# Kernel optimization log

Hardware: AMD Instinct MI355X
Metric: run time of the kernel (lower is better)

The kernel has to match this reference:

```python
import jax, jax.numpy as jnp
import numpy as np

EPS = 1e-6

def _grad_magnitude(x):
    # x: [B, 1, D, H, W]. Valid 3x3x3 conv with shift-subtract kernels:
    # kernel_w differences along D, kernel_d along H, kernel_h along W.
    g_w = x[:, :, 2:, 1:-1, 1:-1] - x[:, :, :-2, 1:-1, 1:-1]
    g_d = x[:, :, 1:-1, 2:, 1:-1] - x[:, :, 1:-1, :-2, 1:-1]
    g_h = x[:, :, 1:-1, 1:-1, 2:] - x[:, :, 1:-1, 1:-1, :-2]
    mag = jnp.sqrt(g_w * g_w + g_d * g_d + g_h * g_h + EPS)
    # replicate-pad back to original spatial size
    return jnp.pad(mag, ((0, 0), (0, 0), (1, 1), (1, 1), (1, 1)), mode='edge')

def setup_inputs() -> dict:
    key = jax.random.key(0)
    k1, k2 = jax.random.split(key)
    shape = (1, 1, 256, 256, 256)
    x1 = jax.random.normal(k1, shape, dtype=jnp.float32)
    x2 = jax.random.normal(k2, shape, dtype=jnp.float32)
    return {"x1": x1, "x2": x2}

def reference(x1, x2):
    g1 = _grad_magnitude(x1)
    g2 = _grad_magnitude(x2)
    return jnp.mean(jnp.abs(g1 - g2))
```

## Files before the change

### kernel.cpp

```cpp
#include <hip/hip_runtime.h>


__global__ __launch_bounds__(256) void grad_loss_kernel(const float* __restrict__ xf1,
                                                        const float* __restrict__ xf2,
                                                        double* __restrict__ acc) {
    const float4* __restrict__ x1 = (const float4*)xf1;
    const float4* __restrict__ x2 = (const float4*)xf2;

    const int tid   = threadIdx.x;
    const int lane  = tid & 63;
    const int hslot = tid >> 6;
    const int htile = blockIdx.x & 63;
    const int dchk  = blockIdx.x >> 6;

    const int h  = 1 + htile * 4 + hslot;
    const int d0 = 1 + dchk * 2;

    const int wbase = 4 * lane;
    const float ww0 = (wbase + 0 == 0)   ? 0.0f : 1.0f;
    const float ww1 = (wbase + 1 == 1)   ? 2.0f : 1.0f;
    const float ww2 = (wbase + 2 == 254) ? 2.0f : 1.0f;
    const float ww3 = (wbase + 3 == 255) ? 0.0f : 1.0f;

    float val = 0.0f;

    if (h <= 254) {
        const float whf = (h == 1 || h == 254) ? 2.0f : 1.0f;
        const int rowbase = h * 64 + lane;
        const int frow    = h * 256 + wbase;

        float4 a1 = x1[(d0 - 1) * 16384 + rowbase];
        float4 b1 = x1[d0 * 16384 + rowbase];
        float4 a2 = x2[(d0 - 1) * 16384 + rowbase];
        float4 b2 = x2[d0 * 16384 + rowbase];

        #pragma unroll
        for (int i = 0; i < 2; ++i) {
            const int d = d0 + i;
            const int base = d * 16384 + rowbase;
            const int fb   = d * 65536 + frow;

            float4 c1 = x1[base + 16384];
            float4 u1 = x1[base - 64];
            float4 v1 = x1[base + 64];
            float  l1 = xf1[fb - 1];
            float  r1 = xf1[fb + 4];
            float4 c2 = x2[base + 16384];
            float4 u2 = x2[base - 64];
            float4 v2 = x2[base + 64];
            float  l2 = xf2[fb - 1];
            float  r2 = xf2[fb + 4];

            float gw, gd, gh;
            gw = c1.x - a1.x; gd = v1.x - u1.x; gh = b1.y - l1;
            float m10 = __builtin_amdgcn_sqrtf(gw * gw + gd * gd + gh * gh + 1e-6f);
            gw = c1.y - a1.y; gd = v1.y - u1.y; gh = b1.z - b1.x;
            float m11 = __builtin_amdgcn_sqrtf(gw * gw + gd * gd + gh * gh + 1e-6f);
            gw = c1.z - a1.z; gd = v1.z - u1.z; gh = b1.w - b1.y;
            float m12 = __builtin_amdgcn_sqrtf(gw * gw + gd * gd + gh * gh + 1e-6f);
            gw = c1.w - a1.w; gd = v1.w - u1.w; gh = r1 - b1.z;
            float m13 = __builtin_amdgcn_sqrtf(gw * gw + gd * gd + gh * gh + 1e-6f);

            gw = c2.x - a2.x; gd = v2.x - u2.x; gh = b2.y - l2;
            float m20 = __builtin_amdgcn_sqrtf(gw * gw + gd * gd + gh * gh + 1e-6f);
            gw = c2.y - a2.y; gd = v2.y - u2.y; gh = b2.z - b2.x;
            float m21 = __builtin_amdgcn_sqrtf(gw * gw + gd * gd + gh * gh + 1e-6f);
            gw = c2.z - a2.z; gd = v2.z - u2.z; gh = b2.w - b2.y;
            float m22 = __builtin_amdgcn_sqrtf(gw * gw + gd * gd + gh * gh + 1e-6f);
            gw = c2.w - a2.w; gd = v2.w - u2.w; gh = r2 - b2.z;
            float m23 = __builtin_amdgcn_sqrtf(gw * gw + gd * gd + gh * gh + 1e-6f);

            float inner = ww0 * fabsf(m10 - m20)
                        + ww1 * fabsf(m11 - m21)
                        + ww2 * fabsf(m12 - m22)
                        + ww3 * fabsf(m13 - m23);

            const float wdf = (d == 1 || d == 254) ? 2.0f : 1.0f;
            val += wdf * whf * inner;

            a1 = b1; b1 = c1;
            a2 = b2; b2 = c2;
        }
    }

    for (int off = 32; off > 0; off >>= 1)
        val += __shfl_down(val, off, 64);

    __shared__ float smem[4];
    const int lid = tid & 63;
    const int wid = tid >> 6;
    if (lid == 0) smem[wid] = val;
    __syncthreads();

    if (wid == 0) {
        float s = (lid < 4) ? smem[lid] : 0.0f;
        s += __shfl_down(s, 2, 64);
        s += __shfl_down(s, 1, 64);
        if (lid == 0)
            atomicAdd(&acc[blockIdx.x & 255], (double)s);
    }
}

__global__ void finalize_kernel(const double* __restrict__ acc, float* __restrict__ out) {
    double v = acc[threadIdx.x];
    for (int off = 32; off > 0; off >>= 1)
        v += __shfl_down(v, off, 64);

    __shared__ double smem[4];
    const int lid = threadIdx.x & 63;
    const int wid = threadIdx.x >> 6;
    if (lid == 0) smem[wid] = v;
    __syncthreads();

    if (threadIdx.x == 0) {
        double s = smem[0] + smem[1] + smem[2] + smem[3];
        out[0] = (float)(s / 16777216.0);
    }
}

extern "C" void kernel_launch(void* const* d_in, const int* in_sizes, int n_in,
                              void* d_out, int out_size, void* d_ws, size_t ws_size,
                              hipStream_t stream) {
    const float* x1 = (const float*)d_in[0];
    const float* x2 = (const float*)d_in[1];
    float* out = (float*)d_out;
    double* acc = (double*)d_ws;

    hipMemsetAsync(d_ws, 0, 256 * sizeof(double), stream);
    grad_loss_kernel<<<64 * 127, 256, 0, stream>>>(x1, x2, acc);
    finalize_kernel<<<1, 256, 0, stream>>>(acc, out);
}
```

Measured before the change: 159.2 us.

## Stage H-neighbour rows in LDS and use shuffles for W halo

```diff
diff --git a/kernel.cpp b/kernel.cpp
--- a/kernel.cpp
+++ b/kernel.cpp
@@ -1,5 +1,7 @@
 #include <hip/hip_runtime.h>
 
+
+#define D_CHUNK 4
 
 __global__ __launch_bounds__(256) void grad_loss_kernel(const float* __restrict__ xf1,
                                                         const float* __restrict__ xf2,
@@ -7,49 +9,76 @@
     const float4* __restrict__ x1 = (const float4*)xf1;
     const float4* __restrict__ x2 = (const float4*)xf2;
 
+    __shared__ float4 plane[2][2][6][64];
+
     const int tid   = threadIdx.x;
     const int lane  = tid & 63;
-    const int hslot = tid >> 6;
+    const int wid   = tid >> 6;
     const int htile = blockIdx.x & 63;
     const int dchk  = blockIdx.x >> 6;
 
-    const int h  = 1 + htile * 4 + hslot;
-    const int d0 = 1 + dchk * 2;
+    const int h0 = 1 + htile * 4;
+    const int d0 = 1 + dchk * D_CHUNK;
 
-    const int wbase = 4 * lane;
-    const float ww0 = (wbase + 0 == 0)   ? 0.0f : 1.0f;
-    const float ww1 = (wbase + 1 == 1)   ? 2.0f : 1.0f;
-    const float ww2 = (wbase + 2 == 254) ? 2.0f : 1.0f;
-    const float ww3 = (wbase + 3 == 255) ? 0.0f : 1.0f;
+    const int  h    = h0 + wid;
+    const bool live = (h <= 254);
+    const int  hrow = (h <= 255) ? h : 255;
+
+    const int halo_row  = (wid < 2) ? (h0 - 1) : ((h0 + 4 <= 255) ? (h0 + 4) : 255);
+    const int halo_slot = (wid < 2) ? 0 : 5;
+    const int halo_inp  = wid & 1;
+    const float4* __restrict__ halo4 = halo_inp ? x2 : x1;
+
+    const int own_f4  = hrow * 64 + lane;
+    const int halo_f4 = halo_row * 64 + lane;
+
+    const float ww0 = (lane == 0)  ? 0.0f : 1.0f;
+    const float ww1 = (lane == 0)  ? 2.0f : 1.0f;
+    const float ww2 = (lane == 63) ? 2.0f : 1.0f;
+    const float ww3 = (lane == 63) ? 0.0f : 1.0f;
+    const float whf = (h == 1 || h == 254) ? 2.0f : 1.0f;
+
+    float4 a1 = x1[(d0 - 1) * 16384 + own_f4];
+    float4 a2 = x2[(d0 - 1) * 16384 + own_f4];
+    float4 b1 = x1[d0 * 16384 + own_f4];
+    float4 b2 = x2[d0 * 16384 + own_f4];
+    float4 hb = halo4[d0 * 16384 + halo_f4];
+    float4 c1 = x1[(d0 + 1) * 16384 + own_f4];
+    float4 c2 = x2[(d0 + 1) * 16384 + own_f4];
+    float4 hc = halo4[(d0 + 1) * 16384 + halo_f4];
+
+    plane[0][0][wid + 1][lane] = b1;
+    plane[0][1][wid + 1][lane] = b2;
+    plane[0][halo_inp][halo_slot][lane] = hb;
+    __syncthreads();
 
     float val = 0.0f;
 
-    if (h <= 254) {
-        const float whf = (h == 1 || h == 254) ? 2.0f : 1.0f;
-        const int rowbase = h * 64 + lane;
-        const int frow    = h * 256 + wbase;
+    #pragma unroll
+    for (int i = 0; i < D_CHUNK; ++i) {
+        const int d   = d0 + i;
+        const int cur = i & 1;
+        const int nxt = cur ^ 1;
+        const int dn  = (d + 2 <= 255) ? (d + 2) : 255;
 
-        float4 a1 = x1[(d0 - 1) * 16384 + rowbase];
-        float4 b1 = x1[d0 * 16384 + rowbase];
-        float4 a2 = x2[(d0 - 1) * 16384 + rowbase];
-        float4 b2 = x2[d0 * 16384 + rowbase];
+        float4 n1 = x1[dn * 16384 + own_f4];
+        float4 n2 = x2[dn * 16384 + own_f4];
+        float4 hn = halo4[dn * 16384 + halo_f4];
 
-        #pragma unroll
-        for (int i = 0; i < 2; ++i) {
-            const int d = d0 + i;
-            const int base = d * 16384 + rowbase;
-            const int fb   = d * 65536 + frow;
+        plane[nxt][0][wid + 1][lane] = c1;
+        plane[nxt][1][wid + 1][lane] = c2;
+        plane[nxt][halo_inp][halo_slot][lane] = hc;
 
-            float4 c1 = x1[base + 16384];
-            float4 u1 = x1[base - 64];
-            float4 v1 = x1[base + 64];
-            float  l1 = xf1[fb - 1];
-            float  r1 = xf1[fb + 4];
-            float4 c2 = x2[base + 16384];
-            float4 u2 = x2[base - 64];
-            float4 v2 = x2[base + 64];
-            float  l2 = xf2[fb - 1];
-            float  r2 = xf2[fb + 4];
+        if (live && d <= 254) {
+            float4 u1 = plane[cur][0][wid][lane];
+            float4 v1 = plane[cur][0][wid + 2][lane];
+            float4 u2 = plane[cur][1][wid][lane];
+            float4 v2 = plane[cur][1][wid + 2][lane];
+
+            float l1 = __shfl_up(b1.w, 1, 64);
+            float r1 = __shfl_down(b1.x, 1, 64);
+            float l2 = __shfl_up(b2.w, 1, 64);
+            float r2 = __shfl_down(b2.x, 1, 64);
 
             float gw, gd, gh;
             gw = c1.x - a1.x; gd = v1.x - u1.x; gh = b1.y - l1;
@@ -77,26 +106,26 @@
 
             const float wdf = (d == 1 || d == 254) ? 2.0f : 1.0f;
             val += wdf * whf * inner;
+        }
 
-            a1 = b1; b1 = c1;
-            a2 = b2; b2 = c2;
-        }
+        a1 = b1; b1 = c1; c1 = n1;
+        a2 = b2; b2 = c2; c2 = n2;
+        hc = hn;
+        __syncthreads();
     }
 
     for (int off = 32; off > 0; off >>= 1)
         val += __shfl_down(val, off, 64);
 
     __shared__ float smem[4];
-    const int lid = tid & 63;
-    const int wid = tid >> 6;
-    if (lid == 0) smem[wid] = val;
+    if (lane == 0) smem[wid] = val;
     __syncthreads();
 
     if (wid == 0) {
-        float s = (lid < 4) ? smem[lid] : 0.0f;
+        float s = (lane < 4) ? smem[lane] : 0.0f;
         s += __shfl_down(s, 2, 64);
         s += __shfl_down(s, 1, 64);
-        if (lid == 0)
+        if (lane == 0)
             atomicAdd(&acc[blockIdx.x & 255], (double)s);
     }
 }
@@ -127,6 +156,6 @@
     double* acc = (double*)d_ws;
 
     hipMemsetAsync(d_ws, 0, 256 * sizeof(double), stream);
-    grad_loss_kernel<<<64 * 127, 256, 0, stream>>>(x1, x2, acc);
+    grad_loss_kernel<<<64 * 64, 256, 0, stream>>>(x1, x2, acc);
     finalize_kernel<<<1, 256, 0, stream>>>(acc, out);
 }
```

Measured after the change: 147.1 us. -7.6%, faster.
